# Performance work log

Hardware: AMD Instinct MI355X
Metric: run time of the kernel (lower is better)

## Reference

```python
import jax, jax.numpy as jnp
import numpy as np

SQ, SK, D = 8192, 8192, 128

def setup_inputs() -> dict:
    k = jax.random.key(0)
    kq, kk, kv = jax.random.split(k, 3)
    query = jax.random.normal(kq, (SQ, D), dtype=jnp.float32)
    key = jax.random.normal(kk, (SK, D), dtype=jnp.float32)
    value = jax.random.normal(kv, (SK, D), dtype=jnp.float32)
    return {"query": query, "key": key, "value": value}

def reference(query, key, value):
    # attn_weights = dot_general(q, k, contract last dims) -> [Sq, Sk]
    attn_weights = jnp.einsum('qd,kd->qk', query, key)
    # softmax over key dims (second half of attn_weights dims)
    attn_weights = jax.nn.softmax(attn_weights, axis=-1)
    # dropout is identity: train=False -> deterministic
    # y = dot_general(attn_weights, value, contract key dims) -> [Sq, Dv]
    y = jnp.einsum('qk,kd->qd', attn_weights, value)
    return y
```

## Files before the change

kernel.cpp:

```cpp
#include <hip/hip_runtime.h>
#include <hip/hip_bf16.h>
#include <stdint.h>

#define SQ 8192
#define SK 8192
#define DH 128
#define NIT 32
#define L2E 1.4426950408889634f
#define CB 40.0f

typedef __attribute__((ext_vector_type(8))) _Float16 f16x8;
typedef __attribute__((ext_vector_type(8))) short bf16x8;
typedef __attribute__((ext_vector_type(16))) float f32x16;
typedef __attribute__((ext_vector_type(4))) short s16x4;

__device__ __forceinline__ short f2h(float f) {
  _Float16 h = (_Float16)f;
  return __builtin_bit_cast(short, h);
}
__device__ __forceinline__ short f2bf(float f) {
  uint32_t u = __builtin_bit_cast(uint32_t, f);
  u = (u + 0x7FFFu + ((u >> 16) & 1u)) >> 16;
  return (short)u;
}

__global__ __launch_bounds__(256) void prep_kernel(const float* __restrict__ K,
                                                   const float* __restrict__ V,
                                                   short* __restrict__ Kimg,
                                                   short* __restrict__ Vimg) {
  __shared__ short T[32][136];
  const int tid = threadIdx.x;
  if (blockIdx.x < 256) {
    const int kb = blockIdx.x;
#pragma unroll
    for (int i = 0; i < 2; ++i) {
      int ci = i * 256 + tid;
      int kc = ci >> 6, lane = ci & 63;
      int key = kb * 32 + (lane & 31);
      int k0 = kc * 16 + (lane >> 5) * 8;
      const float* src = K + (size_t)key * DH + k0;
      float4 a = *(const float4*)src;
      float4 b = *(const float4*)(src + 4);
      s16x4 o0, o1;
      o0.x = f2h(a.x); o0.y = f2h(a.y); o0.z = f2h(a.z); o0.w = f2h(a.w);
      o1.x = f2h(b.x); o1.y = f2h(b.y); o1.z = f2h(b.z); o1.w = f2h(b.w);
      s16x4* dst = (s16x4*)(Kimg + (size_t)kb * 4096 + ci * 8);
      dst[0] = o0; dst[1] = o1;
    }
  } else {
    const int kb = blockIdx.x - 256;
#pragma unroll
    for (int i = 0; i < 4; ++i) {
      int fi = i * 256 + tid;
      int key = fi >> 5;
      int dc = (fi & 31) * 4;
      float4 v = ((const float4*)V)[(size_t)(kb * 32 + key) * (DH / 4) + (fi & 31)];
      T[key][dc + 0] = f2bf(v.x); T[key][dc + 1] = f2bf(v.y);
      T[key][dc + 2] = f2bf(v.z); T[key][dc + 3] = f2bf(v.w);
    }
    __syncthreads();
#pragma unroll
    for (int i = 0; i < 3; ++i) {
      int ci = i * 256 + tid;
      if (ci < 640) {
        int lane = ci & 63;
        int g = ci >> 6;
        int dt = g % 5, ks = g / 5;
        s16x4 o0, o1;
        if (dt == 4) {
          o0.x = o0.y = o0.z = o0.w = (short)0x3F80;
          o1 = o0;
        } else {
          int k0 = ks * 16 + (lane >> 5) * 8;
          int d = dt * 32 + (lane & 31);
          o0.x = T[k0 + 0][d]; o0.y = T[k0 + 1][d];
          o0.z = T[k0 + 2][d]; o0.w = T[k0 + 3][d];
          o1.x = T[k0 + 4][d]; o1.y = T[k0 + 5][d];
          o1.z = T[k0 + 6][d]; o1.w = T[k0 + 7][d];
        }
        s16x4* dst = (s16x4*)(Vimg + (size_t)kb * 5120 + ci * 8);
        dst[0] = o0; dst[1] = o1;
      }
    }
  }
}

__global__ __launch_bounds__(512, 2) void attn_kernel(const float* __restrict__ Q,
                                                      const short* __restrict__ Kimg,
                                                      const short* __restrict__ Vimg,
                                                      float* __restrict__ out) {
  __shared__ __align__(16) char smem[67584];
  short* Psh = (short*)smem;

  const int tid = threadIdx.x;
  const int w = tid >> 6;
  const int lane = tid & 63;
  const int half = lane >> 5;
  const int l32 = lane & 31;
  const int qrow0 = blockIdx.x * 32;

  f16x8 qf[8];
  {
    const float* qp = Q + (size_t)(qrow0 + l32) * DH + half * 8;
#pragma unroll
    for (int kc = 0; kc < 8; ++kc) {
      float4 a = *(const float4*)(qp + kc * 16);
      float4 b = *(const float4*)(qp + kc * 16 + 4);
      f16x8 h;
      h[0] = (_Float16)a.x; h[1] = (_Float16)a.y; h[2] = (_Float16)a.z; h[3] = (_Float16)a.w;
      h[4] = (_Float16)b.x; h[5] = (_Float16)b.y; h[6] = (_Float16)b.z; h[7] = (_Float16)b.w;
      qf[kc] = h;
    }
  }

  f32x16 of[5];
#pragma unroll
  for (int dt = 0; dt < 5; ++dt)
#pragma unroll
    for (int c = 0; c < 16; ++c) of[dt][c] = 0.f;

  f16x8 kf[8];
  bf16x8 vf[10];

  {
    const short* kp = Kimg + (size_t)w * 4096;
    const short* vp = Vimg + (size_t)w * 5120;
#pragma unroll
    for (int kc = 0; kc < 8; ++kc) kf[kc] = *(const f16x8*)(kp + kc * 512 + lane * 8);
#pragma unroll
    for (int g = 0; g < 10; ++g) vf[g] = *(const bf16x8*)(vp + g * 512 + lane * 8);
  }

  for (int t = 0; t < NIT; ++t) {
    f32x16 sacc;
#pragma unroll
    for (int c = 0; c < 16; ++c) sacc[c] = 0.f;
#pragma unroll
    for (int kc = 0; kc < 8; ++kc)
      sacc = __builtin_amdgcn_mfma_f32_32x32x16_f16(qf[kc], kf[kc], sacc, 0, 0, 0);

    if (t + 1 < NIT) {
      const short* kp = Kimg + (size_t)((t + 1) * 8 + w) * 4096;
#pragma unroll
      for (int kc = 0; kc < 8; ++kc) kf[kc] = *(const f16x8*)(kp + kc * 512 + lane * 8);
    }

#pragma unroll
    for (int c = 0; c < 16; ++c) {
      float p = exp2f(fmaf(sacc[c], L2E, -CB));
      int row = (c & 3) + 8 * (c >> 2) + 4 * half;
      Psh[w * 1280 + row * 40 + l32] = f2bf(p);
    }

    asm volatile("s_waitcnt lgkmcnt(0)" ::: "memory");
    bf16x8 pa0 = *(const bf16x8*)(Psh + w * 1280 + l32 * 40 + half * 8);
    bf16x8 pa1 = *(const bf16x8*)(Psh + w * 1280 + l32 * 40 + 16 + half * 8);

#pragma unroll
    for (int dt = 0; dt < 5; ++dt) {
      of[dt] = __builtin_amdgcn_mfma_f32_32x32x16_bf16(pa0, vf[dt], of[dt], 0, 0, 0);
      of[dt] = __builtin_amdgcn_mfma_f32_32x32x16_bf16(pa1, vf[5 + dt], of[dt], 0, 0, 0);
    }

    if (t + 1 < NIT) {
      const short* vp = Vimg + (size_t)((t + 1) * 8 + w) * 5120;
#pragma unroll
      for (int g = 0; g < 10; ++g) vf[g] = *(const bf16x8*)(vp + g * 512 + lane * 8);
    }
  }

  __syncthreads();
  float* mO = (float*)smem;
  float* R = mO + (w & 3) * 4224;
  if (w < 4) {
#pragma unroll
    for (int c = 0; c < 16; ++c) {
      const int row = (c & 3) + 8 * (c >> 2) + 4 * half;
      float* br = R + row * 132;
#pragma unroll
      for (int dt = 0; dt < 4; ++dt) br[dt * 32 + l32] = of[dt][c];
      if (l32 == 0) br[128] = of[4][c];
    }
  }
  __syncthreads();
  if (w >= 4) {
#pragma unroll
    for (int c = 0; c < 16; ++c) {
      const int row = (c & 3) + 8 * (c >> 2) + 4 * half;
      float* br = R + row * 132;
#pragma unroll
      for (int dt = 0; dt < 4; ++dt) br[dt * 32 + l32] += of[dt][c];
      if (l32 == 0) br[128] += of[4][c];
    }
  }
  __syncthreads();
  {
    const int row = tid >> 4;
    const int cg = tid & 15;
    float den = mO[row * 132 + 128] + mO[4224 + row * 132 + 128] +
                mO[8448 + row * 132 + 128] + mO[12672 + row * 132 + 128];
    float inv = 1.f / den;
    float4 s0 = {0.f, 0.f, 0.f, 0.f}, s1 = {0.f, 0.f, 0.f, 0.f};
#pragma unroll
    for (int rg = 0; rg < 4; ++rg) {
      const float* p = mO + rg * 4224 + row * 132 + cg * 8;
      float4 a = *(const float4*)p;
      float4 b = *(const float4*)(p + 4);
      s0.x += a.x; s0.y += a.y; s0.z += a.z; s0.w += a.w;
      s1.x += b.x; s1.y += b.y; s1.z += b.z; s1.w += b.w;
    }
    s0.x *= inv; s0.y *= inv; s0.z *= inv; s0.w *= inv;
    s1.x *= inv; s1.y *= inv; s1.z *= inv; s1.w *= inv;
    float* op = out + (size_t)(qrow0 + row) * DH + cg * 8;
    *(float4*)op = s0;
    *(float4*)(op + 4) = s1;
  }
}

extern "C" void kernel_launch(void* const* d_in, const int* in_sizes, int n_in,
                              void* d_out, int out_size, void* d_ws, size_t ws_size,
                              hipStream_t stream) {
  const float* Q = (const float*)d_in[0];
  const float* K = (const float*)d_in[1];
  const float* V = (const float*)d_in[2];
  float* out = (float*)d_out;
  short* Kimg = (short*)d_ws;
  short* Vimg = (short*)d_ws + (size_t)SK * DH;
  prep_kernel<<<512, 256, 0, stream>>>(K, V, Kimg, Vimg);
  attn_kernel<<<SQ / 32, 512, 0, stream>>>(Q, Kimg, Vimg, out);
}
```

Before: 120.4 us.

## Compute S transposed so P stays in registers; sum denominators in VALU

```diff
diff --git a/kernel.cpp b/kernel.cpp
--- a/kernel.cpp
+++ b/kernel.cpp
@@ -13,6 +13,7 @@
 typedef __attribute__((ext_vector_type(8))) short bf16x8;
 typedef __attribute__((ext_vector_type(16))) float f32x16;
 typedef __attribute__((ext_vector_type(4))) short s16x4;
+typedef __attribute__((ext_vector_type(4))) unsigned int u32x4;
 
 __device__ __forceinline__ short f2h(float f) {
   _Float16 h = (_Float16)f;
@@ -60,27 +61,20 @@
     }
     __syncthreads();
 #pragma unroll
-    for (int i = 0; i < 3; ++i) {
+    for (int i = 0; i < 2; ++i) {
       int ci = i * 256 + tid;
-      if (ci < 640) {
-        int lane = ci & 63;
-        int g = ci >> 6;
-        int dt = g % 5, ks = g / 5;
-        s16x4 o0, o1;
-        if (dt == 4) {
-          o0.x = o0.y = o0.z = o0.w = (short)0x3F80;
-          o1 = o0;
-        } else {
-          int k0 = ks * 16 + (lane >> 5) * 8;
-          int d = dt * 32 + (lane & 31);
-          o0.x = T[k0 + 0][d]; o0.y = T[k0 + 1][d];
-          o0.z = T[k0 + 2][d]; o0.w = T[k0 + 3][d];
-          o1.x = T[k0 + 4][d]; o1.y = T[k0 + 5][d];
-          o1.z = T[k0 + 6][d]; o1.w = T[k0 + 7][d];
-        }
-        s16x4* dst = (s16x4*)(Vimg + (size_t)kb * 5120 + ci * 8);
-        dst[0] = o0; dst[1] = o1;
-      }
+      int lane = ci & 63;
+      int g = ci >> 6;
+      int dt = g & 3, ks = g >> 2;
+      int base = ks * 16 + (lane >> 5) * 4;
+      int d = dt * 32 + (lane & 31);
+      s16x4 o0, o1;
+      o0.x = T[base + 0][d]; o0.y = T[base + 1][d];
+      o0.z = T[base + 2][d]; o0.w = T[base + 3][d];
+      o1.x = T[base + 8][d]; o1.y = T[base + 9][d];
+      o1.z = T[base + 10][d]; o1.w = T[base + 11][d];
+      s16x4* dst = (s16x4*)(Vimg + (size_t)kb * 4096 + ci * 8);
+      dst[0] = o0; dst[1] = o1;
     }
   }
 }
@@ -90,8 +84,6 @@
                                                       const short* __restrict__ Vimg,
                                                       float* __restrict__ out) {
   __shared__ __align__(16) char smem[67584];
-  short* Psh = (short*)smem;
-
   const int tid = threadIdx.x;
   const int w = tid >> 6;
   const int lane = tid & 63;
@@ -113,22 +105,23 @@
     }
   }
 
-  f32x16 of[5];
-#pragma unroll
-  for (int dt = 0; dt < 5; ++dt)
+  f32x16 of[4];
+#pragma unroll
+  for (int dt = 0; dt < 4; ++dt)
 #pragma unroll
     for (int c = 0; c < 16; ++c) of[dt][c] = 0.f;
+  float l_lane = 0.f;
 
   f16x8 kf[8];
-  bf16x8 vf[10];
+  bf16x8 vf[8];
 
   {
     const short* kp = Kimg + (size_t)w * 4096;
-    const short* vp = Vimg + (size_t)w * 5120;
+    const short* vp = Vimg + (size_t)w * 4096;
 #pragma unroll
     for (int kc = 0; kc < 8; ++kc) kf[kc] = *(const f16x8*)(kp + kc * 512 + lane * 8);
 #pragma unroll
-    for (int g = 0; g < 10; ++g) vf[g] = *(const bf16x8*)(vp + g * 512 + lane * 8);
+    for (int g = 0; g < 8; ++g) vf[g] = *(const bf16x8*)(vp + g * 512 + lane * 8);
   }
 
   for (int t = 0; t < NIT; ++t) {
@@ -137,7 +130,7 @@
     for (int c = 0; c < 16; ++c) sacc[c] = 0.f;
 #pragma unroll
     for (int kc = 0; kc < 8; ++kc)
-      sacc = __builtin_amdgcn_mfma_f32_32x32x16_f16(qf[kc], kf[kc], sacc, 0, 0, 0);
+      sacc = __builtin_amdgcn_mfma_f32_32x32x16_f16(kf[kc], qf[kc], sacc, 0, 0, 0);
 
     if (t + 1 < NIT) {
       const short* kp = Kimg + (size_t)((t + 1) * 8 + w) * 4096;
@@ -145,29 +138,38 @@
       for (int kc = 0; kc < 8; ++kc) kf[kc] = *(const f16x8*)(kp + kc * 512 + lane * 8);
     }
 
-#pragma unroll
-    for (int c = 0; c < 16; ++c) {
-      float p = exp2f(fmaf(sacc[c], L2E, -CB));
-      int row = (c & 3) + 8 * (c >> 2) + 4 * half;
-      Psh[w * 1280 + row * 40 + l32] = f2bf(p);
-    }
-
-    asm volatile("s_waitcnt lgkmcnt(0)" ::: "memory");
-    bf16x8 pa0 = *(const bf16x8*)(Psh + w * 1280 + l32 * 40 + half * 8);
-    bf16x8 pa1 = *(const bf16x8*)(Psh + w * 1280 + l32 * 40 + 16 + half * 8);
-
-#pragma unroll
-    for (int dt = 0; dt < 5; ++dt) {
+    u32x4 pav0, pav1;
+#pragma unroll
+    for (int r = 0; r < 4; ++r) {
+      float pA = __builtin_amdgcn_exp2f(fmaf(sacc[2 * r], L2E, -CB));
+      float pB = __builtin_amdgcn_exp2f(fmaf(sacc[2 * r + 1], L2E, -CB));
+      float pC = __builtin_amdgcn_exp2f(fmaf(sacc[8 + 2 * r], L2E, -CB));
+      float pD = __builtin_amdgcn_exp2f(fmaf(sacc[8 + 2 * r + 1], L2E, -CB));
+      l_lane += (pA + pB) + (pC + pD);
+      uint32_t uA = __builtin_bit_cast(uint32_t, pA); uA += 0x7FFFu + ((uA >> 16) & 1u);
+      uint32_t uB = __builtin_bit_cast(uint32_t, pB); uB += 0x7FFFu + ((uB >> 16) & 1u);
+      uint32_t uC = __builtin_bit_cast(uint32_t, pC); uC += 0x7FFFu + ((uC >> 16) & 1u);
+      uint32_t uD = __builtin_bit_cast(uint32_t, pD); uD += 0x7FFFu + ((uD >> 16) & 1u);
+      pav0[r] = __builtin_amdgcn_perm(uB, uA, 0x07060302u);
+      pav1[r] = __builtin_amdgcn_perm(uD, uC, 0x07060302u);
+    }
+    bf16x8 pa0 = __builtin_bit_cast(bf16x8, pav0);
+    bf16x8 pa1 = __builtin_bit_cast(bf16x8, pav1);
+
+#pragma unroll
+    for (int dt = 0; dt < 4; ++dt) {
       of[dt] = __builtin_amdgcn_mfma_f32_32x32x16_bf16(pa0, vf[dt], of[dt], 0, 0, 0);
-      of[dt] = __builtin_amdgcn_mfma_f32_32x32x16_bf16(pa1, vf[5 + dt], of[dt], 0, 0, 0);
+      of[dt] = __builtin_amdgcn_mfma_f32_32x32x16_bf16(pa1, vf[4 + dt], of[dt], 0, 0, 0);
     }
 
     if (t + 1 < NIT) {
-      const short* vp = Vimg + (size_t)((t + 1) * 8 + w) * 5120;
-#pragma unroll
-      for (int g = 0; g < 10; ++g) vf[g] = *(const bf16x8*)(vp + g * 512 + lane * 8);
-    }
-  }
+      const short* vp = Vimg + (size_t)((t + 1) * 8 + w) * 4096;
+#pragma unroll
+      for (int g = 0; g < 8; ++g) vf[g] = *(const bf16x8*)(vp + g * 512 + lane * 8);
+    }
+  }
+
+  float l_tot = l_lane + __shfl_xor(l_lane, 32);
 
   __syncthreads();
   float* mO = (float*)smem;
@@ -179,8 +181,8 @@
       float* br = R + row * 132;
 #pragma unroll
       for (int dt = 0; dt < 4; ++dt) br[dt * 32 + l32] = of[dt][c];
-      if (l32 == 0) br[128] = of[4][c];
-    }
+    }
+    if (half == 0) R[l32 * 132 + 128] = l_tot;
   }
   __syncthreads();
   if (w >= 4) {
@@ -190,8 +192,8 @@
       float* br = R + row * 132;
 #pragma unroll
       for (int dt = 0; dt < 4; ++dt) br[dt * 32 + l32] += of[dt][c];
-      if (l32 == 0) br[128] += of[4][c];
-    }
+    }
+    if (half == 0) R[l32 * 132 + 128] += l_tot;
   }
   __syncthreads();
   {
```

New measurement: 112.7 us. 6.5% less time.
